# Optimization experiments

Measured on AMD Instinct MI355X. Metric: run time of the kernel, lower is better.

## Reference

```python
import jax, jax.numpy as jnp
import numpy as np

EPS = 1e-9


def setup_inputs() -> dict:
    key = jax.random.key(0)
    kx, kw = jax.random.split(key)
    B, S, D, E = 4, 4096, 4096, 64
    x = jax.random.normal(kx, (B, S, D), dtype=jnp.float32)
    # nn.Linear(d_model, num_experts, bias=False): weight shape (E, D)
    W_gate = jax.random.normal(kw, (E, D), dtype=jnp.float32) * (1.0 / np.sqrt(D))
    return {"x": x, "W_gate": W_gate}


def reference(x, W_gate):
    # logits: (B, S, E) = x @ W_gate^T
    logits = jnp.einsum("bsd,ed->bse", x, W_gate)
    probs = jax.nn.softmax(logits, axis=-1)
    top_k = 2
    weights, indices = jax.lax.top_k(probs, top_k)  # (B, S, K) each
    weights = weights / (jnp.sum(weights, axis=-1, keepdims=True) + EPS)
    return indices, weights, logits
```

## Files before the change

kernel.cpp:

```cpp
#include <hip/hip_runtime.h>
#include <math.h>

#define TOKENS 16384
#define DD 4096
#define NE 64
#define MBLK 128
#define KB 16

#define GLDS16(gp, lp) __builtin_amdgcn_global_load_lds((gp), (lp), 16, 0, 0)

__global__ void k0_transpose(const float* __restrict__ Wg, float* __restrict__ WT) {
  const int k0 = blockIdx.x * 64;
  const int e  = threadIdx.x & 63;
  const int kq = threadIdx.x >> 6;
#pragma unroll
  for (int kk = 0; kk < 16; ++kk) {
    const int k = k0 + kq * 16 + kk;
    WT[(long)k * NE + e] = Wg[(long)e * DD + k];
  }
}

__global__ __launch_bounds__(256, 4)
void k1_gemm(const float* __restrict__ x, const float* __restrict__ WT,
             float* __restrict__ part, int kPerSlice) {
  __shared__ __align__(16) float xs[2][MBLK * KB];
  __shared__ __align__(16) float wt[2][KB * NE];

  const int nm   = TOKENS / MBLK;
  const int mblk = blockIdx.x % nm;
  const int s    = blockIdx.x / nm;
  const int tid  = threadIdx.x;
  const int lane = tid & 63;
  const int wid  = tid >> 6;
  const long t0  = (long)mblk * MBLK;
  const int k0   = s * kPerSlice;

  const int eg   = lane & 7;
  const int tg   = lane >> 3;
  const int tokb = wid * 32 + tg * 4;
  const int eoff = eg * 8;
  const int xkey = tg & 3;

  const float* gxs[2];
#pragma unroll
  for (int q = 0; q < 2; ++q) {
    const int tok = (wid * 2 + q) * 16 + (lane >> 2);
    const int kk  = ((lane & 3) ^ ((tok >> 2) & 3)) << 2;
    gxs[q] = x + (t0 + tok) * (long)DD + k0 + kk;
  }
  const float* gw = WT + (long)(k0 + wid * 4 + (lane >> 4)) * NE + (lane & 15) * 4;

  float acc[4][8];
#pragma unroll
  for (int i = 0; i < 4; ++i)
#pragma unroll
    for (int j = 0; j < 8; ++j) acc[i][j] = 0.f;

  const int nchunk = kPerSlice / KB;

#pragma unroll
  for (int q = 0; q < 2; ++q) GLDS16(gxs[q], &xs[0][(wid * 2 + q) * 256]);
  GLDS16(gw, &wt[0][wid * 256]);

  int cur = 0;
  for (int c = 0; c < nchunk; ++c) {
    __syncthreads();

    if (c + 1 < nchunk) {
      const int nb = cur ^ 1;
      const long go = (long)(c + 1) * KB;
#pragma unroll
      for (int q = 0; q < 2; ++q)
        GLDS16(gxs[q] + go, &xs[nb][(wid * 2 + q) * 256]);
      GLDS16(gw + go * NE, &wt[nb][wid * 256]);
    }

#pragma unroll
    for (int kkc = 0; kkc < 4; ++kkc) {
      float4 xv[4];
#pragma unroll
      for (int i = 0; i < 4; ++i)
        xv[i] = *(const float4*)&xs[cur][(tokb + i) * KB + ((kkc ^ xkey) << 2)];
#pragma unroll
      for (int m = 0; m < 4; ++m) {
        const int kk = kkc * 4 + m;
        const float4 w0 = *(const float4*)&wt[cur][kk * NE + eoff];
        const float4 w1 = *(const float4*)&wt[cur][kk * NE + eoff + 4];
#pragma unroll
        for (int i = 0; i < 4; ++i) {
          const float xm = (&xv[i].x)[m];
          acc[i][0] += xm * w0.x; acc[i][1] += xm * w0.y;
          acc[i][2] += xm * w0.z; acc[i][3] += xm * w0.w;
          acc[i][4] += xm * w1.x; acc[i][5] += xm * w1.y;
          acc[i][6] += xm * w1.z; acc[i][7] += xm * w1.w;
        }
      }
    }
    cur ^= 1;
  }

  float* pb = part + ((long)s * TOKENS + t0 + tokb) * NE + eoff;
#pragma unroll
  for (int i = 0; i < 4; ++i) {
    float* pr = pb + (long)i * NE;
    *(float4*)(pr)     = make_float4(acc[i][0], acc[i][1], acc[i][2], acc[i][3]);
    *(float4*)(pr + 4) = make_float4(acc[i][4], acc[i][5], acc[i][6], acc[i][7]);
  }
}

__global__ __launch_bounds__(256)
void k2_finish(const float* __restrict__ part, int S, float* __restrict__ out) {
  const int tid  = threadIdx.x;
  const int lane = tid & 63;
  const int wv   = tid >> 6;
  const long t   = (long)blockIdx.x * 4 + wv;

  const float* p = part + t * NE + lane;
  float logit = 0.f;
  for (int s = 0; s < S; ++s) logit += p[(long)s * TOKENS * NE];

  out[4 * TOKENS + t * NE + lane] = logit;

  float v = logit; int i = lane;
#pragma unroll
  for (int off = 32; off; off >>= 1) {
    float ov = __shfl_xor(v, off);
    int   oi = __shfl_xor(i, off);
    if (ov > v || (ov == v && oi < i)) { v = ov; i = oi; }
  }
  const float m = v; const int i1 = i;

  float vv = (lane == i1) ? -INFINITY : logit; int ii = lane;
#pragma unroll
  for (int off = 32; off; off >>= 1) {
    float ov = __shfl_xor(vv, off);
    int   oi = __shfl_xor(ii, off);
    if (ov > vv || (ov == vv && oi < ii)) { vv = ov; ii = oi; }
  }
  const int i2 = ii;

  float z = expf(logit - m);
  float Z = z;
#pragma unroll
  for (int off = 32; off; off >>= 1) Z += __shfl_xor(Z, off);

  float p1 = __shfl(z, i1) / Z;
  float p2 = __shfl(z, i2) / Z;

  if (lane == 0) {
    float denom = p1 + p2 + 1e-9f;
    out[t * 2 + 0] = (float)i1;
    out[t * 2 + 1] = (float)i2;
    out[2 * TOKENS + t * 2 + 0] = p1 / denom;
    out[2 * TOKENS + t * 2 + 1] = p2 / denom;
  }
}

extern "C" void kernel_launch(void* const* d_in, const int* in_sizes, int n_in,
                              void* d_out, int out_size, void* d_ws, size_t ws_size,
                              hipStream_t stream) {
  const float* x  = (const float*)d_in[0];
  const float* Wg = (const float*)d_in[1];
  float* out = (float*)d_out;

  float* WT = (float*)d_ws;
  const size_t wtBytes    = (size_t)DD * NE * sizeof(float);
  const size_t sliceBytes = (size_t)TOKENS * NE * sizeof(float);

  int S = 8;
  while (S > 1 && wtBytes + (size_t)S * sliceBytes > ws_size) S >>= 1;
  float* part = (float*)((char*)d_ws + wtBytes);
  if (wtBytes + sliceBytes > ws_size) {
    S = 1;
    part = out + 4 * TOKENS;
  }
  const int kPerSlice = DD / S;

  k0_transpose<<<dim3(DD / 64), 256, 0, stream>>>(Wg, WT);
  k1_gemm<<<dim3((TOKENS / MBLK) * S), 256, 0, stream>>>(x, WT, part, kPerSlice);
  k2_finish<<<dim3(TOKENS / 4), 256, 0, stream>>>(part, S, out);
}
```

Measured before the change: 406.8 us.

## Double token block and widen per-thread expert tile with broadcast weight reads

Token block per workgroup grows from 128 to 256, and each thread now computes 4 tokens by 16 experts instead of 4 by 8. Each wave owns a 16-expert slice, so weight reads from shared memory are uniform across the wave (broadcast), and each x read feeds twice as many FMAs. This cuts LDS traffic per FMA, and the x swizzle is rebuilt to match the new per-lane row reads. The cost is higher register pressure and LDS use, with launch bounds lowered to 2 blocks per CU and fewer total blocks.

```diff
diff --git a/kernel.cpp b/kernel.cpp
--- a/kernel.cpp
+++ b/kernel.cpp
@@ -4,7 +4,7 @@
 #define TOKENS 16384
 #define DD 4096
 #define NE 64
-#define MBLK 128
+#define MBLK 256
 #define KB 16
 
 #define GLDS16(gp, lp) __builtin_amdgcn_global_load_lds((gp), (lp), 16, 0, 0)
@@ -20,7 +20,7 @@
   }
 }
 
-__global__ __launch_bounds__(256, 4)
+__global__ __launch_bounds__(256, 2)
 void k1_gemm(const float* __restrict__ x, const float* __restrict__ WT,
              float* __restrict__ part, int kPerSlice) {
   __shared__ __align__(16) float xs[2][MBLK * KB];
@@ -35,31 +35,28 @@
   const long t0  = (long)mblk * MBLK;
   const int k0   = s * kPerSlice;
 
-  const int eg   = lane & 7;
-  const int tg   = lane >> 3;
-  const int tokb = wid * 32 + tg * 4;
-  const int eoff = eg * 8;
-  const int xkey = tg & 3;
+  const int we0   = wid * 16;
+  const int rdkey = (lane & 3) ^ ((lane >> 2) & 3);
 
-  const float* gxs[2];
+  const int gkey = ((lane >> 2) & 3) ^ ((lane >> 4) & 3);
+  const float* gxs[4];
 #pragma unroll
-  for (int q = 0; q < 2; ++q) {
-    const int tok = (wid * 2 + q) * 16 + (lane >> 2);
-    const int kk  = ((lane & 3) ^ ((tok >> 2) & 3)) << 2;
-    gxs[q] = x + (t0 + tok) * (long)DD + k0 + kk;
+  for (int q = 0; q < 4; ++q) {
+    const int tok = wid * 64 + q * 16 + (lane >> 2);
+    gxs[q] = x + (t0 + tok) * (long)DD + k0 + (((lane & 3) ^ gkey) << 2);
   }
   const float* gw = WT + (long)(k0 + wid * 4 + (lane >> 4)) * NE + (lane & 15) * 4;
 
-  float acc[4][8];
+  float acc[4][16];
 #pragma unroll
   for (int i = 0; i < 4; ++i)
 #pragma unroll
-    for (int j = 0; j < 8; ++j) acc[i][j] = 0.f;
+    for (int j = 0; j < 16; ++j) acc[i][j] = 0.f;
 
   const int nchunk = kPerSlice / KB;
 
 #pragma unroll
-  for (int q = 0; q < 2; ++q) GLDS16(gxs[q], &xs[0][(wid * 2 + q) * 256]);
+  for (int q = 0; q < 4; ++q) GLDS16(gxs[q], &xs[0][wid * 1024 + q * 256]);
   GLDS16(gw, &wt[0][wid * 256]);
 
   int cur = 0;
@@ -70,41 +67,50 @@
       const int nb = cur ^ 1;
       const long go = (long)(c + 1) * KB;
 #pragma unroll
-      for (int q = 0; q < 2; ++q)
-        GLDS16(gxs[q] + go, &xs[nb][(wid * 2 + q) * 256]);
+      for (int q = 0; q < 4; ++q)
+        GLDS16(gxs[q] + go, &xs[nb][wid * 1024 + q * 256]);
       GLDS16(gw + go * NE, &wt[nb][wid * 256]);
     }
 
 #pragma unroll
     for (int kkc = 0; kkc < 4; ++kkc) {
+      const int sl = (kkc ^ rdkey) << 2;
       float4 xv[4];
 #pragma unroll
       for (int i = 0; i < 4; ++i)
-        xv[i] = *(const float4*)&xs[cur][(tokb + i) * KB + ((kkc ^ xkey) << 2)];
+        xv[i] = *(const float4*)&xs[cur][lane * 16 + i * 1024 + sl];
 #pragma unroll
       for (int m = 0; m < 4; ++m) {
         const int kk = kkc * 4 + m;
-        const float4 w0 = *(const float4*)&wt[cur][kk * NE + eoff];
-        const float4 w1 = *(const float4*)&wt[cur][kk * NE + eoff + 4];
+        const float4 w0 = *(const float4*)&wt[cur][kk * NE + we0];
+        const float4 w1 = *(const float4*)&wt[cur][kk * NE + we0 + 4];
+        const float4 w2 = *(const float4*)&wt[cur][kk * NE + we0 + 8];
+        const float4 w3 = *(const float4*)&wt[cur][kk * NE + we0 + 12];
 #pragma unroll
         for (int i = 0; i < 4; ++i) {
           const float xm = (&xv[i].x)[m];
-          acc[i][0] += xm * w0.x; acc[i][1] += xm * w0.y;
-          acc[i][2] += xm * w0.z; acc[i][3] += xm * w0.w;
-          acc[i][4] += xm * w1.x; acc[i][5] += xm * w1.y;
-          acc[i][6] += xm * w1.z; acc[i][7] += xm * w1.w;
+          acc[i][0]  += xm * w0.x; acc[i][1]  += xm * w0.y;
+          acc[i][2]  += xm * w0.z; acc[i][3]  += xm * w0.w;
+          acc[i][4]  += xm * w1.x; acc[i][5]  += xm * w1.y;
+          acc[i][6]  += xm * w1.z; acc[i][7]  += xm * w1.w;
+          acc[i][8]  += xm * w2.x; acc[i][9]  += xm * w2.y;
+          acc[i][10] += xm * w2.z; acc[i][11] += xm * w2.w;
+          acc[i][12] += xm * w3.x; acc[i][13] += xm * w3.y;
+          acc[i][14] += xm * w3.z; acc[i][15] += xm * w3.w;
         }
       }
     }
     cur ^= 1;
   }
 
-  float* pb = part + ((long)s * TOKENS + t0 + tokb) * NE + eoff;
+  float* pb = part + ((long)s * TOKENS + t0 + lane) * NE + we0;
 #pragma unroll
   for (int i = 0; i < 4; ++i) {
-    float* pr = pb + (long)i * NE;
-    *(float4*)(pr)     = make_float4(acc[i][0], acc[i][1], acc[i][2], acc[i][3]);
-    *(float4*)(pr + 4) = make_float4(acc[i][4], acc[i][5], acc[i][6], acc[i][7]);
+    float* pr = pb + (long)(64 * i) * NE;
+    *(float4*)(pr)      = make_float4(acc[i][0],  acc[i][1],  acc[i][2],  acc[i][3]);
+    *(float4*)(pr + 4)  = make_float4(acc[i][4],  acc[i][5],  acc[i][6],  acc[i][7]);
+    *(float4*)(pr + 8)  = make_float4(acc[i][8],  acc[i][9],  acc[i][10], acc[i][11]);
+    *(float4*)(pr + 12) = make_float4(acc[i][12], acc[i][13], acc[i][14], acc[i][15]);
   }
 }
 
```

After: 413.4 us. Within noise of the previous version (+1.6%).
